# Kernel tuning notes

Measured on AMD Instinct MI355X. Metric: run time of the kernel, lower is better.

The kernel has to match this reference:

```python
import jax, jax.numpy as jnp
import numpy as np

ALPHA = 1.702
LIMIT = 7.0


def setup_inputs() -> dict:
    key = jax.random.key(0)
    ks = jax.random.split(key, 7)
    T, K, E, H, I = 512, 2, 32, 512, 512
    bf16 = jnp.bfloat16
    x = jax.random.normal(ks[0], (T, H), dtype=jnp.float32).astype(bf16)
    expert_indices = jax.random.randint(ks[1], (T, K), 0, E, dtype=jnp.int32)
    expert_weights = jax.random.uniform(ks[2], (T, K), dtype=jnp.float32).astype(bf16)
    mlp1_weight = (jax.random.normal(ks[3], (E, 2 * I, H), dtype=jnp.float32) * 0.02).astype(bf16)
    mlp1_bias = (jax.random.normal(ks[4], (E, 2 * I), dtype=jnp.float32) * 0.02).astype(bf16)
    mlp2_weight = (jax.random.normal(ks[5], (E, H, I), dtype=jnp.float32) * 0.02).astype(bf16)
    mlp2_bias = (jax.random.normal(ks[6], (E, H), dtype=jnp.float32) * 0.02).astype(bf16)
    return {
        "x": x,
        "expert_indices": expert_indices,
        "expert_weights": expert_weights,
        "mlp1_weight": mlp1_weight,
        "mlp1_bias": mlp1_bias,
        "mlp2_weight": mlp2_weight,
        "mlp2_bias": mlp2_bias,
    }


def _swiglu_fused(t):
    # t: (tokens, k, 2*I) interleaved; even cols -> gate, odd cols -> linear
    x_glu = jnp.minimum(t[..., ::2], jnp.asarray(LIMIT, t.dtype))
    x_lin = jnp.clip(t[..., 1::2], -LIMIT, LIMIT)
    out_glu = x_glu * jax.nn.sigmoid(jnp.asarray(ALPHA, t.dtype) * x_glu)
    return out_glu * (x_lin + 1)


def reference(x, expert_indices, expert_weights, mlp1_weight, mlp1_bias, mlp2_weight, mlp2_bias):
    # Naive per-token gather of full expert weights, as in the original module.
    w1 = mlp1_weight[expert_indices]            # (b, e, 2I, H)
    b1 = mlp1_bias[expert_indices]              # (b, e, 2I)
    t = jnp.einsum('beck,bk->bec', w1, x) + b1  # (b, e, 2I)
    t = _swiglu_fused(t)                        # (b, e, I)
    w2 = mlp2_weight[expert_indices]            # (b, e, H, I)
    b2 = mlp2_bias[expert_indices]              # (b, e, H)
    t = jnp.einsum('beck,bek->bec', w2, t) + b2  # (b, e, H)
    return jnp.einsum('bec,be->bc', t, expert_weights)  # (b, H)
```

## Files before the change

### kernel.cpp

```cpp
#include <hip/hip_runtime.h>
#include <hip/hip_bf16.h>
#include <cstdint>


#define MOE_E 32
#define MOE_H 512
#define MOE_I 512
#define MOE_2I 1024
#define MOE_CAP 1024

typedef __attribute__((ext_vector_type(8))) short s16x8;
typedef __attribute__((ext_vector_type(4))) float f32x4;

#define GLDS16(g, l)  __builtin_amdgcn_global_load_lds(                        \
    (const __attribute__((address_space(1))) unsigned int*)(g),                \
    (__attribute__((address_space(3))) unsigned int*)(l), 16, 0, 0)

__device__ __forceinline__ s16x8 pack8(float4 f0, float4 f1) {
    union { unsigned int u[4]; s16x8 v; } r;
    r.u[0] = (__float_as_uint(f0.y) & 0xFFFF0000u) | (__float_as_uint(f0.x) >> 16);
    r.u[1] = (__float_as_uint(f0.w) & 0xFFFF0000u) | (__float_as_uint(f0.z) >> 16);
    r.u[2] = (__float_as_uint(f1.y) & 0xFFFF0000u) | (__float_as_uint(f1.x) >> 16);
    r.u[3] = (__float_as_uint(f1.w) & 0xFFFF0000u) | (__float_as_uint(f1.z) >> 16);
    return r.v;
}

__global__ __launch_bounds__(1024) void moe_route(const int* __restrict__ idx,
                                                  int* __restrict__ cnt,
                                                  int* __restrict__ lists) {
    __shared__ int scnt[MOE_E];
    const int p = threadIdx.x;
    if (p < MOE_E) scnt[p] = 0;
    __syncthreads();
    int e = idx[p];
    e = (e < 0) ? 0 : (e > MOE_E - 1 ? MOE_E - 1 : e);
    const int pos = atomicAdd(&scnt[e], 1);
    lists[e * MOE_CAP + pos] = p;
    __syncthreads();
    if (p < MOE_E) cnt[p] = scnt[p];
}

__global__ __launch_bounds__(256) void moe_mlp1(
    const float* __restrict__ x, const float* __restrict__ w1,
    const float* __restrict__ b1, const int* __restrict__ cnt,
    const int* __restrict__ lists, float* __restrict__ t1p) {
    __shared__ float Bs[32 * 64 * 4];
    __shared__ float As[32 * 32 * 4];
    const int e = blockIdx.y;
    const int ne = cnt[e];
    if (ne == 0) return;
    const int kz = blockIdx.z;
    const int tid  = threadIdx.x;
    const int lane = tid & 63;
    const int wave = tid >> 6;
    const int n16  = lane & 15;
    const int k8   = lane >> 4;
    const int* lst = lists + e * MOE_CAP;
    const int cg = blockIdx.x * 64 + wave * 16 + n16;
    const float bv = (kz == 0) ? b1[e * MOE_2I + cg] : 0.0f;
    const float* wbase = w1 + ((size_t)e * MOE_2I + blockIdx.x * 64) * MOE_H
                         + kz * 128;
    float* t1 = t1p + (size_t)kz * MOE_CAP * MOE_2I;

    #pragma unroll
    for (int j = 0; j < 8; ++j) {
        const int u = (j * 4 + wave) * 64 + lane;
        const int q = u >> 6, r = u & 63;
        GLDS16(wbase + (size_t)r * MOE_H + q * 4, Bs + (size_t)(j * 4 + wave) * 256);
    }

    for (int m0 = 0; m0 < ne; m0 += 32) {
        __syncthreads();
        #pragma unroll
        for (int j = 0; j < 4; ++j) {
            const int u = (j * 4 + wave) * 64 + lane;
            const int q = u >> 5, r = u & 31;
            const int pm = lst[min(m0 + r, ne - 1)];
            GLDS16(x + (size_t)(pm >> 1) * MOE_H + kz * 128 + q * 4,
                   As + (size_t)(j * 4 + wave) * 256);
        }
        __syncthreads();

        f32x4 acc0 = {0.f, 0.f, 0.f, 0.f};
        f32x4 acc1 = {0.f, 0.f, 0.f, 0.f};
        #pragma unroll
        for (int ks = 0; ks < 4; ++ks) {
            const int qB = ks * 8 + k8 * 2;
            const float4 B0  = *(const float4*)(Bs + 4 * (qB * 64 + wave * 16 + n16));
            const float4 B1  = *(const float4*)(Bs + 4 * ((qB + 1) * 64 + wave * 16 + n16));
            const float4 A00 = *(const float4*)(As + 4 * (qB * 32 + n16));
            const float4 A01 = *(const float4*)(As + 4 * ((qB + 1) * 32 + n16));
            const float4 A10 = *(const float4*)(As + 4 * (qB * 32 + 16 + n16));
            const float4 A11 = *(const float4*)(As + 4 * ((qB + 1) * 32 + 16 + n16));
            const s16x8 BF = pack8(B0, B1);
            acc0 = __builtin_amdgcn_mfma_f32_16x16x32_bf16(pack8(A00, A01), BF, acc0, 0, 0, 0);
            acc1 = __builtin_amdgcn_mfma_f32_16x16x32_bf16(pack8(A10, A11), BF, acc1, 0, 0, 0);
        }
        const int mend = ne - m0;
        #pragma unroll
        for (int tile = 0; tile < 2; ++tile) {
            const f32x4 acc = tile ? acc1 : acc0;
            #pragma unroll
            for (int q = 0; q < 4; ++q) {
                const int mrow = tile * 16 + k8 * 4 + q;
                if (mrow < mend) {
                    const int p = lst[m0 + mrow];
                    t1[(size_t)p * MOE_2I + cg] = acc[q] + bv;
                }
            }
        }
    }
}

__global__ __launch_bounds__(256) void moe_swiglu(
    const float* __restrict__ t1p, float* __restrict__ hbuf) {
    const int tid  = threadIdx.x;
    const int pair = blockIdx.x * 2 + (tid >> 7);
    const int i0   = (tid & 127) * 4;
    float4 s0 = {0.f, 0.f, 0.f, 0.f}, s1 = {0.f, 0.f, 0.f, 0.f};
    #pragma unroll
    for (int kzi = 0; kzi < 4; ++kzi) {
        const float* b = t1p + (size_t)kzi * MOE_CAP * MOE_2I
                       + (size_t)pair * MOE_2I + i0 * 2;
        const float4 v0 = *(const float4*)b;
        const float4 v1 = *(const float4*)(b + 4);
        s0.x += v0.x; s0.y += v0.y; s0.z += v0.z; s0.w += v0.w;
        s1.x += v1.x; s1.y += v1.y; s1.z += v1.z; s1.w += v1.w;
    }
    float g0 = s0.x, l0 = s0.y, g1 = s0.z, l1 = s0.w;
    float g2 = s1.x, l2 = s1.y, g3 = s1.z, l3 = s1.w;
    g0 = fminf(g0, 7.0f); l0 = fminf(fmaxf(l0, -7.0f), 7.0f);
    g1 = fminf(g1, 7.0f); l1 = fminf(fmaxf(l1, -7.0f), 7.0f);
    g2 = fminf(g2, 7.0f); l2 = fminf(fmaxf(l2, -7.0f), 7.0f);
    g3 = fminf(g3, 7.0f); l3 = fminf(fmaxf(l3, -7.0f), 7.0f);
    float4 h;
    h.x = g0 / (1.0f + expf(-1.702f * g0)) * (l0 + 1.0f);
    h.y = g1 / (1.0f + expf(-1.702f * g1)) * (l1 + 1.0f);
    h.z = g2 / (1.0f + expf(-1.702f * g2)) * (l2 + 1.0f);
    h.w = g3 / (1.0f + expf(-1.702f * g3)) * (l3 + 1.0f);
    *(float4*)(hbuf + (size_t)pair * MOE_I + i0) = h;
}

__global__ __launch_bounds__(256) void moe_mlp2(
    const float* __restrict__ hbuf, const float* __restrict__ w2,
    const float* __restrict__ b2, const int* __restrict__ cnt,
    const int* __restrict__ lists, float* __restrict__ pop) {
    __shared__ float Bs[32 * 64 * 4];
    __shared__ float As[32 * 32 * 4];
    const int e = blockIdx.y;
    const int ne = cnt[e];
    if (ne == 0) return;
    const int kz = blockIdx.z;
    const int tid  = threadIdx.x;
    const int lane = tid & 63;
    const int wave = tid >> 6;
    const int n16  = lane & 15;
    const int k8   = lane >> 4;
    const int* lst = lists + e * MOE_CAP;
    const int c = blockIdx.x * 64 + wave * 16 + n16;
    const float bv = (kz == 0) ? b2[e * MOE_H + c] : 0.0f;
    const float* wbase = w2 + ((size_t)e * MOE_H + blockIdx.x * 64) * MOE_I
                         + kz * 128;
    float* po = pop + (size_t)kz * MOE_CAP * MOE_H;

    #pragma unroll
    for (int j = 0; j < 8; ++j) {
        const int u = (j * 4 + wave) * 64 + lane;
        const int q = u >> 6, r = u & 63;
        GLDS16(wbase + (size_t)r * MOE_I + q * 4, Bs + (size_t)(j * 4 + wave) * 256);
    }

    for (int m0 = 0; m0 < ne; m0 += 32) {
        __syncthreads();
        #pragma unroll
        for (int j = 0; j < 4; ++j) {
            const int u = (j * 4 + wave) * 64 + lane;
            const int q = u >> 5, r = u & 31;
            const int pm = lst[min(m0 + r, ne - 1)];
            GLDS16(hbuf + (size_t)pm * MOE_I + kz * 128 + q * 4,
                   As + (size_t)(j * 4 + wave) * 256);
        }
        __syncthreads();

        f32x4 acc0 = {0.f, 0.f, 0.f, 0.f};
        f32x4 acc1 = {0.f, 0.f, 0.f, 0.f};
        #pragma unroll
        for (int ks = 0; ks < 4; ++ks) {
            const int qB = ks * 8 + k8 * 2;
            const float4 B0  = *(const float4*)(Bs + 4 * (qB * 64 + wave * 16 + n16));
            const float4 B1  = *(const float4*)(Bs + 4 * ((qB + 1) * 64 + wave * 16 + n16));
            const float4 A00 = *(const float4*)(As + 4 * (qB * 32 + n16));
            const float4 A01 = *(const float4*)(As + 4 * ((qB + 1) * 32 + n16));
            const float4 A10 = *(const float4*)(As + 4 * (qB * 32 + 16 + n16));
            const float4 A11 = *(const float4*)(As + 4 * ((qB + 1) * 32 + 16 + n16));
            const s16x8 BF = pack8(B0, B1);
            acc0 = __builtin_amdgcn_mfma_f32_16x16x32_bf16(pack8(A00, A01), BF, acc0, 0, 0, 0);
            acc1 = __builtin_amdgcn_mfma_f32_16x16x32_bf16(pack8(A10, A11), BF, acc1, 0, 0, 0);
        }
        const int mend = ne - m0;
        #pragma unroll
        for (int tile = 0; tile < 2; ++tile) {
            const f32x4 acc = tile ? acc1 : acc0;
            #pragma unroll
            for (int q = 0; q < 4; ++q) {
                const int mrow = tile * 16 + k8 * 4 + q;
                if (mrow < mend) {
                    const int p = lst[m0 + mrow];
                    po[(size_t)p * MOE_H + c] = acc[q] + bv;
                }
            }
        }
    }
}

__global__ __launch_bounds__(256) void MoEMLPFused_74191265071207_kernel(
    const float* __restrict__ pop, const float* __restrict__ ew,
    float* __restrict__ out) {
    const int o = blockIdx.x * 256 + threadIdx.x;
    const int t = o >> 9;
    const int c = o & 511;
    float s0 = 0.f, s1 = 0.f;
    #pragma unroll
    for (int kzi = 0; kzi < 4; ++kzi) {
        const float* pb = pop + (size_t)kzi * MOE_CAP * MOE_H;
        s0 += pb[(size_t)(2 * t + 0) * MOE_H + c];
        s1 += pb[(size_t)(2 * t + 1) * MOE_H + c];
    }
    out[o] = ew[2 * t + 0] * s0 + ew[2 * t + 1] * s1;
}

extern "C" void kernel_launch(void* const* d_in, const int* in_sizes, int n_in,
                              void* d_out, int out_size, void* d_ws, size_t ws_size,
                              hipStream_t stream) {
    const float* x   = (const float*)d_in[0];
    const int*   idx = (const int*)d_in[1];
    const float* ew  = (const float*)d_in[2];
    const float* w1  = (const float*)d_in[3];
    const float* b1  = (const float*)d_in[4];
    const float* w2  = (const float*)d_in[5];
    const float* b2  = (const float*)d_in[6];
    float* out = (float*)d_out;

    char* ws = (char*)d_ws;
    int* cnt    = (int*)ws;
    int* lists  = (int*)(ws + 256);
    float* t1p  = (float*)(ws + 256 + MOE_E * MOE_CAP * 4);
    float* hbuf = t1p + 4u * MOE_CAP * MOE_2I;
    float* pop  = hbuf + (size_t)MOE_CAP * MOE_I;

    moe_route<<<1, 1024, 0, stream>>>(idx, cnt, lists);
    moe_mlp1<<<dim3(16, MOE_E, 4), 256, 0, stream>>>(x, w1, b1, cnt, lists, t1p);
    moe_swiglu<<<512, 256, 0, stream>>>(t1p, hbuf);
    moe_mlp2<<<dim3(8, MOE_E, 4), 256, 0, stream>>>(hbuf, w2, b2, cnt, lists, pop);
    MoEMLPFused_74191265071207_kernel<<<(512 * MOE_H) / 256, 256, 0, stream>>>(
        pop, ew, out);
}
```

Measured before the change: 59.27 us.

## Fuse SwiGLU into MLP1 epilogue, drop split-K partials, store hidden as bf16

Removes the 4-way split-K over the hidden dimension. Each block now loops over K chunks itself, so the partial buffers and their reduction passes go away. SwiGLU is applied in the MLP1 epilogue by pairing gate and linear columns with a lane shuffle, and the result is stored as bf16, which drops the separate swiglu kernel and halves the hidden-buffer traffic. The cost is 4x fewer blocks in each GEMM, which lowers parallelism. Weight tiles are also now reloaded for every 32-token group instead of being loaded once per block.

Result: slower. 62.64 us (+5.7%).

```diff
diff --git a/kernel.cpp b/kernel.cpp
--- a/kernel.cpp
+++ b/kernel.cpp
@@ -11,6 +11,7 @@
 
 typedef __attribute__((ext_vector_type(8))) short s16x8;
 typedef __attribute__((ext_vector_type(4))) float f32x4;
+typedef unsigned short u16;
 
 #define GLDS16(g, l)  __builtin_amdgcn_global_load_lds(                        \
     (const __attribute__((address_space(1))) unsigned int*)(g),                \
@@ -23,6 +24,11 @@
     r.u[2] = (__float_as_uint(f1.y) & 0xFFFF0000u) | (__float_as_uint(f1.x) >> 16);
     r.u[3] = (__float_as_uint(f1.w) & 0xFFFF0000u) | (__float_as_uint(f1.z) >> 16);
     return r.v;
+}
+
+__device__ __forceinline__ u16 f2bf_rtne(float f) {
+    const unsigned int u = __float_as_uint(f);
+    return (u16)((u + 0x7FFFu + ((u >> 16) & 1u)) >> 16);
 }
 
 __global__ __launch_bounds__(1024) void moe_route(const int* __restrict__ idx,
@@ -43,13 +49,12 @@
 __global__ __launch_bounds__(256) void moe_mlp1(
     const float* __restrict__ x, const float* __restrict__ w1,
     const float* __restrict__ b1, const int* __restrict__ cnt,
-    const int* __restrict__ lists, float* __restrict__ t1p) {
-    __shared__ float Bs[32 * 64 * 4];
-    __shared__ float As[32 * 32 * 4];
+    const int* __restrict__ lists, u16* __restrict__ hbuf) {
+    __shared__ float Bs[2048 * 4];
+    __shared__ float As[1024 * 4];
     const int e = blockIdx.y;
     const int ne = cnt[e];
     if (ne == 0) return;
-    const int kz = blockIdx.z;
     const int tid  = threadIdx.x;
     const int lane = tid & 63;
     const int wave = tid >> 6;
@@ -57,100 +62,74 @@
     const int k8   = lane >> 4;
     const int* lst = lists + e * MOE_CAP;
     const int cg = blockIdx.x * 64 + wave * 16 + n16;
-    const float bv = (kz == 0) ? b1[e * MOE_2I + cg] : 0.0f;
-    const float* wbase = w1 + ((size_t)e * MOE_2I + blockIdx.x * 64) * MOE_H
-                         + kz * 128;
-    float* t1 = t1p + (size_t)kz * MOE_CAP * MOE_2I;
-
-    #pragma unroll
-    for (int j = 0; j < 8; ++j) {
-        const int u = (j * 4 + wave) * 64 + lane;
-        const int q = u >> 6, r = u & 63;
-        GLDS16(wbase + (size_t)r * MOE_H + q * 4, Bs + (size_t)(j * 4 + wave) * 256);
-    }
-
-    for (int m0 = 0; m0 < ne; m0 += 32) {
-        __syncthreads();
-        #pragma unroll
-        for (int j = 0; j < 4; ++j) {
-            const int u = (j * 4 + wave) * 64 + lane;
-            const int q = u >> 5, r = u & 31;
-            const int pm = lst[min(m0 + r, ne - 1)];
-            GLDS16(x + (size_t)(pm >> 1) * MOE_H + kz * 128 + q * 4,
-                   As + (size_t)(j * 4 + wave) * 256);
-        }
-        __syncthreads();
-
+    const float bv = b1[e * MOE_2I + cg];
+    const float* wbase = w1 + ((size_t)e * MOE_2I + blockIdx.x * 64) * MOE_H;
+
+    for (int g0 = 0; g0 < ne; g0 += 32) {
         f32x4 acc0 = {0.f, 0.f, 0.f, 0.f};
         f32x4 acc1 = {0.f, 0.f, 0.f, 0.f};
-        #pragma unroll
-        for (int ks = 0; ks < 4; ++ks) {
-            const int qB = ks * 8 + k8 * 2;
-            const float4 B0  = *(const float4*)(Bs + 4 * (qB * 64 + wave * 16 + n16));
-            const float4 B1  = *(const float4*)(Bs + 4 * ((qB + 1) * 64 + wave * 16 + n16));
-            const float4 A00 = *(const float4*)(As + 4 * (qB * 32 + n16));
-            const float4 A01 = *(const float4*)(As + 4 * ((qB + 1) * 32 + n16));
-            const float4 A10 = *(const float4*)(As + 4 * (qB * 32 + 16 + n16));
-            const float4 A11 = *(const float4*)(As + 4 * ((qB + 1) * 32 + 16 + n16));
-            const s16x8 BF = pack8(B0, B1);
-            acc0 = __builtin_amdgcn_mfma_f32_16x16x32_bf16(pack8(A00, A01), BF, acc0, 0, 0, 0);
-            acc1 = __builtin_amdgcn_mfma_f32_16x16x32_bf16(pack8(A10, A11), BF, acc1, 0, 0, 0);
-        }
-        const int mend = ne - m0;
+        for (int kc = 0; kc < 4; ++kc) {
+            __syncthreads();
+            #pragma unroll
+            for (int j = 0; j < 8; ++j) {
+                const int u = (j * 4 + wave) * 64 + lane;
+                const int q = u >> 6, r = u & 63;
+                GLDS16(wbase + (size_t)r * MOE_H + kc * 128 + q * 4,
+                       Bs + (size_t)(j * 4 + wave) * 256);
+            }
+            #pragma unroll
+            for (int j = 0; j < 4; ++j) {
+                const int u = (j * 4 + wave) * 64 + lane;
+                const int q = u >> 5, r = u & 31;
+                const int pm = lst[min(g0 + r, ne - 1)];
+                GLDS16(x + (size_t)(pm >> 1) * MOE_H + kc * 128 + q * 4,
+                       As + (size_t)(j * 4 + wave) * 256);
+            }
+            __syncthreads();
+
+            #pragma unroll
+            for (int ks = 0; ks < 4; ++ks) {
+                const int qB = ks * 8 + k8 * 2;
+                const float4 B0 = *(const float4*)(Bs + 4 * (qB * 64 + wave * 16 + n16));
+                const float4 B1 = *(const float4*)(Bs + 4 * ((qB + 1) * 64 + wave * 16 + n16));
+                const s16x8 BF = pack8(B0, B1);
+                const float4 A00 = *(const float4*)(As + 4 * (qB * 32 + n16));
+                const float4 A01 = *(const float4*)(As + 4 * ((qB + 1) * 32 + n16));
+                acc0 = __builtin_amdgcn_mfma_f32_16x16x32_bf16(pack8(A00, A01), BF, acc0, 0, 0, 0);
+                const float4 A10 = *(const float4*)(As + 4 * (qB * 32 + 16 + n16));
+                const float4 A11 = *(const float4*)(As + 4 * ((qB + 1) * 32 + 16 + n16));
+                acc1 = __builtin_amdgcn_mfma_f32_16x16x32_bf16(pack8(A10, A11), BF, acc1, 0, 0, 0);
+            }
+        }
         #pragma unroll
         for (int tile = 0; tile < 2; ++tile) {
             const f32x4 acc = tile ? acc1 : acc0;
             #pragma unroll
             for (int q = 0; q < 4; ++q) {
-                const int mrow = tile * 16 + k8 * 4 + q;
-                if (mrow < mend) {
-                    const int p = lst[m0 + mrow];
-                    t1[(size_t)p * MOE_2I + cg] = acc[q] + bv;
+                const float val = acc[q] + bv;
+                const float other = __shfl_xor(val, 1);
+                const int mrow = g0 + tile * 16 + k8 * 4 + q;
+                if ((cg & 1) == 0 && mrow < ne) {
+                    const float g = fminf(val, 7.0f);
+                    const float l = fminf(fmaxf(other, -7.0f), 7.0f);
+                    const float h = g / (1.0f + expf(-1.702f * g)) * (l + 1.0f);
+                    const int p = lst[mrow];
+                    hbuf[(size_t)p * MOE_I + (cg >> 1)] = f2bf_rtne(h);
                 }
             }
         }
     }
 }
 
-__global__ __launch_bounds__(256) void moe_swiglu(
-    const float* __restrict__ t1p, float* __restrict__ hbuf) {
-    const int tid  = threadIdx.x;
-    const int pair = blockIdx.x * 2 + (tid >> 7);
-    const int i0   = (tid & 127) * 4;
-    float4 s0 = {0.f, 0.f, 0.f, 0.f}, s1 = {0.f, 0.f, 0.f, 0.f};
-    #pragma unroll
-    for (int kzi = 0; kzi < 4; ++kzi) {
-        const float* b = t1p + (size_t)kzi * MOE_CAP * MOE_2I
-                       + (size_t)pair * MOE_2I + i0 * 2;
-        const float4 v0 = *(const float4*)b;
-        const float4 v1 = *(const float4*)(b + 4);
-        s0.x += v0.x; s0.y += v0.y; s0.z += v0.z; s0.w += v0.w;
-        s1.x += v1.x; s1.y += v1.y; s1.z += v1.z; s1.w += v1.w;
-    }
-    float g0 = s0.x, l0 = s0.y, g1 = s0.z, l1 = s0.w;
-    float g2 = s1.x, l2 = s1.y, g3 = s1.z, l3 = s1.w;
-    g0 = fminf(g0, 7.0f); l0 = fminf(fmaxf(l0, -7.0f), 7.0f);
-    g1 = fminf(g1, 7.0f); l1 = fminf(fmaxf(l1, -7.0f), 7.0f);
-    g2 = fminf(g2, 7.0f); l2 = fminf(fmaxf(l2, -7.0f), 7.0f);
-    g3 = fminf(g3, 7.0f); l3 = fminf(fmaxf(l3, -7.0f), 7.0f);
-    float4 h;
-    h.x = g0 / (1.0f + expf(-1.702f * g0)) * (l0 + 1.0f);
-    h.y = g1 / (1.0f + expf(-1.702f * g1)) * (l1 + 1.0f);
-    h.z = g2 / (1.0f + expf(-1.702f * g2)) * (l2 + 1.0f);
-    h.w = g3 / (1.0f + expf(-1.702f * g3)) * (l3 + 1.0f);
-    *(float4*)(hbuf + (size_t)pair * MOE_I + i0) = h;
-}
-
 __global__ __launch_bounds__(256) void moe_mlp2(
-    const float* __restrict__ hbuf, const float* __restrict__ w2,
+    const u16* __restrict__ hbuf, const float* __restrict__ w2,
     const float* __restrict__ b2, const int* __restrict__ cnt,
-    const int* __restrict__ lists, float* __restrict__ pop) {
-    __shared__ float Bs[32 * 64 * 4];
-    __shared__ float As[32 * 32 * 4];
+    const int* __restrict__ lists, float* __restrict__ po) {
+    __shared__ float Bs[2048 * 4];
+    __shared__ u16 As[512 * 8];
     const int e = blockIdx.y;
     const int ne = cnt[e];
     if (ne == 0) return;
-    const int kz = blockIdx.z;
     const int tid  = threadIdx.x;
     const int lane = tid & 63;
     const int wave = tid >> 6;
@@ -158,54 +137,52 @@
     const int k8   = lane >> 4;
     const int* lst = lists + e * MOE_CAP;
     const int c = blockIdx.x * 64 + wave * 16 + n16;
-    const float bv = (kz == 0) ? b2[e * MOE_H + c] : 0.0f;
-    const float* wbase = w2 + ((size_t)e * MOE_H + blockIdx.x * 64) * MOE_I
-                         + kz * 128;
-    float* po = pop + (size_t)kz * MOE_CAP * MOE_H;
-
-    #pragma unroll
-    for (int j = 0; j < 8; ++j) {
-        const int u = (j * 4 + wave) * 64 + lane;
-        const int q = u >> 6, r = u & 63;
-        GLDS16(wbase + (size_t)r * MOE_I + q * 4, Bs + (size_t)(j * 4 + wave) * 256);
-    }
-
-    for (int m0 = 0; m0 < ne; m0 += 32) {
-        __syncthreads();
-        #pragma unroll
-        for (int j = 0; j < 4; ++j) {
-            const int u = (j * 4 + wave) * 64 + lane;
-            const int q = u >> 5, r = u & 31;
-            const int pm = lst[min(m0 + r, ne - 1)];
-            GLDS16(hbuf + (size_t)pm * MOE_I + kz * 128 + q * 4,
-                   As + (size_t)(j * 4 + wave) * 256);
-        }
-        __syncthreads();
-
+    const float bv = b2[e * MOE_H + c];
+    const float* wbase = w2 + ((size_t)e * MOE_H + blockIdx.x * 64) * MOE_I;
+
+    for (int g0 = 0; g0 < ne; g0 += 32) {
         f32x4 acc0 = {0.f, 0.f, 0.f, 0.f};
         f32x4 acc1 = {0.f, 0.f, 0.f, 0.f};
-        #pragma unroll
-        for (int ks = 0; ks < 4; ++ks) {
-            const int qB = ks * 8 + k8 * 2;
-            const float4 B0  = *(const float4*)(Bs + 4 * (qB * 64 + wave * 16 + n16));
-            const float4 B1  = *(const float4*)(Bs + 4 * ((qB + 1) * 64 + wave * 16 + n16));
-            const float4 A00 = *(const float4*)(As + 4 * (qB * 32 + n16));
-            const float4 A01 = *(const float4*)(As + 4 * ((qB + 1) * 32 + n16));
-            const float4 A10 = *(const float4*)(As + 4 * (qB * 32 + 16 + n16));
-            const float4 A11 = *(const float4*)(As + 4 * ((qB + 1) * 32 + 16 + n16));
-            const s16x8 BF = pack8(B0, B1);
-            acc0 = __builtin_amdgcn_mfma_f32_16x16x32_bf16(pack8(A00, A01), BF, acc0, 0, 0, 0);
-            acc1 = __builtin_amdgcn_mfma_f32_16x16x32_bf16(pack8(A10, A11), BF, acc1, 0, 0, 0);
-        }
-        const int mend = ne - m0;
+        for (int kc = 0; kc < 4; ++kc) {
+            __syncthreads();
+            #pragma unroll
+            for (int j = 0; j < 8; ++j) {
+                const int u = (j * 4 + wave) * 64 + lane;
+                const int q = u >> 6, r = u & 63;
+                GLDS16(wbase + (size_t)r * MOE_I + kc * 128 + q * 4,
+                       Bs + (size_t)(j * 4 + wave) * 256);
+            }
+            #pragma unroll
+            for (int j = 0; j < 2; ++j) {
+                const int u = (j * 4 + wave) * 64 + lane;
+                const int q = u >> 5, r = u & 31;
+                const int pm = lst[min(g0 + r, ne - 1)];
+                GLDS16(hbuf + (size_t)pm * MOE_I + kc * 128 + q * 8,
+                       As + (size_t)(j * 4 + wave) * 512);
+            }
+            __syncthreads();
+
+            #pragma unroll
+            for (int ks = 0; ks < 4; ++ks) {
+                const int qB = ks * 8 + k8 * 2;
+                const float4 B0 = *(const float4*)(Bs + 4 * (qB * 64 + wave * 16 + n16));
+                const float4 B1 = *(const float4*)(Bs + 4 * ((qB + 1) * 64 + wave * 16 + n16));
+                const s16x8 BF = pack8(B0, B1);
+                const int uA = (ks * 4 + k8) * 32;
+                const s16x8 A0 = *(const s16x8*)(As + (size_t)(uA + n16) * 8);
+                const s16x8 A1 = *(const s16x8*)(As + (size_t)(uA + 16 + n16) * 8);
+                acc0 = __builtin_amdgcn_mfma_f32_16x16x32_bf16(A0, BF, acc0, 0, 0, 0);
+                acc1 = __builtin_amdgcn_mfma_f32_16x16x32_bf16(A1, BF, acc1, 0, 0, 0);
+            }
+        }
         #pragma unroll
         for (int tile = 0; tile < 2; ++tile) {
             const f32x4 acc = tile ? acc1 : acc0;
             #pragma unroll
             for (int q = 0; q < 4; ++q) {
-                const int mrow = tile * 16 + k8 * 4 + q;
-                if (mrow < mend) {
-                    const int p = lst[m0 + mrow];
+                const int mrow = g0 + tile * 16 + k8 * 4 + q;
+                if (mrow < ne) {
+                    const int p = lst[mrow];
                     po[(size_t)p * MOE_H + c] = acc[q] + bv;
                 }
             }
@@ -214,19 +191,13 @@
 }
 
 __global__ __launch_bounds__(256) void MoEMLPFused_74191265071207_kernel(
-    const float* __restrict__ pop, const float* __restrict__ ew,
+    const float* __restrict__ po, const float* __restrict__ ew,
     float* __restrict__ out) {
     const int o = blockIdx.x * 256 + threadIdx.x;
     const int t = o >> 9;
     const int c = o & 511;
-    float s0 = 0.f, s1 = 0.f;
-    #pragma unroll
-    for (int kzi = 0; kzi < 4; ++kzi) {
-        const float* pb = pop + (size_t)kzi * MOE_CAP * MOE_H;
-        s0 += pb[(size_t)(2 * t + 0) * MOE_H + c];
-        s1 += pb[(size_t)(2 * t + 1) * MOE_H + c];
-    }
-    out[o] = ew[2 * t + 0] * s0 + ew[2 * t + 1] * s1;
+    out[o] = ew[2 * t + 0] * po[(size_t)(2 * t + 0) * MOE_H + c]
+           + ew[2 * t + 1] * po[(size_t)(2 * t + 1) * MOE_H + c];
 }
 
 extern "C" void kernel_launch(void* const* d_in, const int* in_sizes, int n_in,
@@ -242,16 +213,14 @@
     float* out = (float*)d_out;
 
     char* ws = (char*)d_ws;
-    int* cnt    = (int*)ws;
-    int* lists  = (int*)(ws + 256);
-    float* t1p  = (float*)(ws + 256 + MOE_E * MOE_CAP * 4);
-    float* hbuf = t1p + 4u * MOE_CAP * MOE_2I;
-    float* pop  = hbuf + (size_t)MOE_CAP * MOE_I;
+    int* cnt   = (int*)ws;
+    int* lists = (int*)(ws + 256);
+    u16* hbuf  = (u16*)(ws + 256 + MOE_E * MOE_CAP * 4);
+    float* po  = (float*)((char*)hbuf + (size_t)MOE_CAP * MOE_I * 2);
 
     moe_route<<<1, 1024, 0, stream>>>(idx, cnt, lists);
-    moe_mlp1<<<dim3(16, MOE_E, 4), 256, 0, stream>>>(x, w1, b1, cnt, lists, t1p);
-    moe_swiglu<<<512, 256, 0, stream>>>(t1p, hbuf);
-    moe_mlp2<<<dim3(8, MOE_E, 4), 256, 0, stream>>>(hbuf, w2, b2, cnt, lists, pop);
+    moe_mlp1<<<dim3(16, MOE_E), 256, 0, stream>>>(x, w1, b1, cnt, lists, hbuf);
+    moe_mlp2<<<dim3(8, MOE_E), 256, 0, stream>>>(hbuf, w2, b2, cnt, lists, po);
     MoEMLPFused_74191265071207_kernel<<<(512 * MOE_H) / 256, 256, 0, stream>>>(
-        pop, ew, out);
-}
+        po, ew, out);
+}
```
